# Kernel optimization log

Hardware: AMD Instinct MI355X
Metric: run time of the kernel (lower is better)

Reference implementation:

```python
import jax, jax.numpy as jnp
import numpy as np

# Model constants matching init_kwargs
C1, C2, FS, IMG = 1024, 3, 16, 128
NF = FS * FS                     # n_features = 256 (== pos_out_dim)
L = C1 // NF                     # 4 hypernetwork-generated layers
WD = NF + (L - 1) * NF + L       # weight_dim = 1028
M = NF // 4                      # 64 frequencies per coord dim
SIGMA = 10.0
B = 8


def _coords_pe(b):
    """get_coords([IMG, IMG]) + positional_encoding, flattened to [b, IMG*IMG, NF]."""
    v0, v1 = -0.99999, 1.0
    r = (v1 - v0) / (2 * IMG)
    seq = v0 + r + 2 * r * jnp.arange(IMG, dtype=jnp.float32)
    gy, gx = jnp.meshgrid(seq, seq, indexing='ij')
    coords = jnp.stack([gy, gx], axis=-1)                 # [IMG, IMG, 2]
    j = jnp.arange(M, dtype=jnp.float32)
    coeffs = 2.0 * jnp.pi * (SIGMA ** (j / M))            # [M]
    vp = coeffs * coords[..., None]                       # [IMG, IMG, 2, M]
    pe = jnp.concatenate([jnp.cos(vp), jnp.sin(vp)], -1)  # [IMG, IMG, 2, 2M]
    pe = pe.reshape(IMG, IMG, 4 * M)                      # flatten(-2,-1)
    x2 = pe.reshape(1, IMG * IMG, NF)
    return jnp.broadcast_to(x2, (b, IMG * IMG, NF))


def setup_inputs() -> dict:
    key = jax.random.key(0)
    ks = jax.random.split(key, 5)
    std = 0.001  # matches _initialize_weights
    x = jax.random.normal(ks[0], (B, C1, FS, FS), jnp.float32)
    conv_w = std * jax.random.normal(ks[1], (C1 + L, C1), jnp.float32)  # 1x1 conv kernel
    conv_b = jnp.zeros((C1 + L,), jnp.float32)
    wfine_w = std * jax.random.normal(ks[2], (NF, NF), jnp.float32)
    wfine_b = jnp.zeros((NF,), jnp.float32)
    last1_w = std * jax.random.normal(ks[3], (C2, NF), jnp.float32)
    last1_b = jnp.zeros((C2,), jnp.float32)
    prelu_a = jnp.array(0.25, jnp.float32)  # nn.PReLU default single param
    return {"x": x, "conv_w": conv_w, "conv_b": conv_b,
            "wfine_w": wfine_w, "wfine_b": wfine_b,
            "last1_w": last1_w, "last1_b": last1_b, "prelu_a": prelu_a}


def reference(x, conv_w, conv_b, wfine_w, wfine_b, last1_w, last1_b, prelu_a):
    b = x.shape[0]
    x2 = _coords_pe(b)  # [b, N_px, NF]
    # 1x1 conv == channel matmul
    x1 = jnp.einsum('bchw,oc->bohw', x, conv_w) + conv_b[None, :, None, None]
    W = x1.reshape(b, WD, NF)
    W = jnp.einsum('bik,jk->bij', W, wfine_w) + wfine_b  # W_fine linear
    out = x2
    for j in range(L):
        wj = W[:, NF * j + j: NF * (j + 1) + j, :]           # [b, NF, NF]
        bj = W[:, NF * (j + 1) + j: NF * (j + 1) + j + 1, :]  # [b, 1, NF]
        h = jnp.einsum('bij,bjk->bik', out, wj) + bj
        out = jnp.where(h >= 0, h, prelu_a * h)              # PReLU
    out = jnp.einsum('bik,ck->bic', out, last1_w) + last1_b  # last1
    out = jax.nn.silu(out)                                   # SiLU
    out = out.transpose(0, 2, 1).reshape(b, C2, IMG, IMG)
    return out
```

## Files before the change

kernel.cpp:

```cpp
#include <hip/hip_runtime.h>
#include <hip/hip_fp16.h>
#include <math.h>

typedef _Float16 f16;
typedef _Float16 f16x4 __attribute__((ext_vector_type(4)));
typedef _Float16 f16x8 __attribute__((ext_vector_type(8)));
typedef float f32x4 __attribute__((ext_vector_type(4)));

#define MFMA16(a, b, c) __builtin_amdgcn_mfma_f32_16x16x32_f16((a), (b), (c), 0, 0, 0)

static constexpr float SW_W    = 1024.f;
static constexpr float SA_A    = 64.f;
static constexpr float INV_SW  = 1.f / 1024.f;
static constexpr float INV_SW2 = 1.f / (1024.f * 1024.f);
static constexpr float INV_SASW = 1.f / (64.f * 1024.f);

static constexpr size_t OFF_CY = 0;
static constexpr size_t OFF_CX = OFF_CY + 65536;
static constexpr size_t OFF_LW = OFF_CX + 65536;
static constexpr size_t OFF_S  = OFF_LW + 8192;
static constexpr size_t OFF_CW = OFF_S  + 1024;
static constexpr size_t OFF_M2 = OFF_CW + (size_t)1088 * 1024 * 2;
static constexpr size_t OFF_W  = OFF_M2 + (size_t)8 * 256 * 1024 * 2;
static constexpr size_t OFF_AY = OFF_W  + (size_t)8 * 1028 * 256 * 4;
static constexpr size_t OFF_BX = OFF_AY + (size_t)8 * 128 * 256 * 2;
static constexpr size_t OFF_WT = OFF_BX + (size_t)8 * 128 * 256 * 2;

static __device__ inline f32x4 zero4() { f32x4 v = {0.f, 0.f, 0.f, 0.f}; return v; }

__global__ __launch_bounds__(256, 4) void k_prepA(
    const float* __restrict__ x, const float* __restrict__ wfine,
    f16* __restrict__ M2,
    float* __restrict__ cy, float* __restrict__ cx,
    f16* __restrict__ lwf, const float* __restrict__ lw,
    const float* __restrict__ cw, f16* __restrict__ cw16,
    float* __restrict__ S)
{
    __shared__ __align__(16) f16 Ab[2][64 * 32];
    __shared__ __align__(16) f16 Bb[2][64 * 32];
    const int bid = blockIdx.x;
    const int t = threadIdx.x;
    if (bid < 512) {
        const int lane = t & 63;
        const int wc = t >> 6;
        const int nlo = lane & 15, q4 = lane >> 4;
        const int b = bid >> 6, rem = bid & 63;
        const int jt = rem >> 4, ct = rem & 15;
        const int j0 = jt << 6, c0 = ct << 6;

        auto stageA = [&](int buf, int k0) {
            const float* src = x + (((size_t)((b << 10) + c0 + (t >> 2))) << 8) + k0 + ((t & 3) << 3);
            f16x8 v;
            #pragma unroll
            for (int i = 0; i < 8; i++) v[i] = (f16)src[i];
            *(f16x8*)(&Ab[buf][t << 3]) = v;
        };
        auto stageB = [&](int buf, int k0) {
            const float* src = wfine + (size_t)(j0 + (t >> 2)) * 256 + k0 + ((t & 3) << 3);
            f16x8 v;
            #pragma unroll
            for (int i = 0; i < 8; i++) v[i] = (f16)(src[i] * SW_W);
            *(f16x8*)(&Bb[buf][t << 3]) = v;
        };

        f32x4 acc[4];
        #pragma unroll
        for (int mt = 0; mt < 4; mt++) acc[mt] = zero4();

        stageA(0, 0); stageB(0, 0);
        __syncthreads();
        for (int c = 0; c < 8; c++) {
            const int cb = c & 1;
            if (c + 1 < 8) { stageA(cb ^ 1, (c + 1) << 5); stageB(cb ^ 1, (c + 1) << 5); }
            f16x8 af[4], bf;
            bf = *(const f16x8*)(&Bb[cb][(((wc << 4) + nlo) << 5) + (q4 << 3)]);
            #pragma unroll
            for (int mt = 0; mt < 4; mt++)
                af[mt] = *(const f16x8*)(&Ab[cb][(((mt << 4) + nlo) << 5) + (q4 << 3)]);
            #pragma unroll
            for (int mt = 0; mt < 4; mt++)
                acc[mt] = MFMA16(af[mt], bf, acc[mt]);
            __syncthreads();
        }
        const int j = j0 + (wc << 4) + nlo;
        #pragma unroll
        for (int mt = 0; mt < 4; mt++) {
            const int cc = c0 + (mt << 4) + (q4 << 2);
            f16x4 pk;
            #pragma unroll
            for (int i = 0; i < 4; i++) pk[i] = (f16)acc[mt][i];
            *(f16x4*)(M2 + (((size_t)((b << 8) + j)) << 10) + cc) = pk;
        }
        return;
    }
    if (bid < 642) {
        int id = (bid - 512) * 256 + t;
        const float r = 1.99999f / 256.f;
        if (id < 32768) {
            float* dst = (id < 16384) ? cy : cx;
            int e = id & 16383;
            int row = e >> 7, f = e & 127;
            float s = -0.99999f + r + 2.f * r * (float)row;
            float coef = 6.283185307179586f * powf(10.f, (float)(f & 63) * (1.f / 64.f));
            float arg = coef * s;
            dst[e] = (f < 64) ? cosf(arg) : sinf(arg);
        } else {
            int id2 = id - 32768;
            int c = id2 >> 6, lane = id2 & 63;
            int nlo = lane & 15, q4 = lane >> 4;
            f16x8 v;
            #pragma unroll
            for (int ko = 0; ko < 8; ko++)
                v[ko] = (nlo < 3) ? (f16)(lw[nlo * 256 + (c << 5) + (q4 << 3) + ko] * SW_W) : (f16)0.f;
            *(f16x8*)(lwf + id2 * 8) = v;
        }
        return;
    }
    if (bid < 1186) {
        const int g8 = (bid - 642) * 256 + t;
        const int row = g8 >> 7, col0 = (g8 & 127) << 3;
        f16x8 v;
        if (row < 1028) {
            const float* src = cw + (size_t)row * 1024 + col0;
            #pragma unroll
            for (int i = 0; i < 8; i++) v[i] = (f16)(src[i] * SW_W);
        } else {
            #pragma unroll
            for (int i = 0; i < 8; i++) v[i] = (f16)0.f;
        }
        *(f16x8*)(cw16 + (size_t)g8 * 8) = v;
        return;
    }
    {
        const float* src = wfine + (size_t)t * 256;
        float s = 0.f;
        for (int k = 0; k < 256; k += 4) {
            const f32x4 v = *(const f32x4*)(src + k);
            s += (v[0] + v[1]) + (v[2] + v[3]);
        }
        S[t] = s;
    }
}

__global__ __launch_bounds__(256, 4) void k_gemmB(
    const f16* __restrict__ cw16, const f16* __restrict__ M2,
    const float* __restrict__ conv_b, const float* __restrict__ S,
    const float* __restrict__ wfine_b, float* __restrict__ W)
{
    __shared__ __align__(16) f16 Ab[2][64 * 32];
    __shared__ __align__(16) f16 Bb[2][64 * 32];
    const int t = threadIdx.x;
    const int lane = t & 63;
    const int wc = t >> 6;
    const int nlo = lane & 15, q4 = lane >> 4;
    const int blk = blockIdx.x;
    const int b = blk / 68, rem = blk % 68;
    const int it = rem >> 2, jt = rem & 3;
    const int i0 = it << 6, j0 = jt << 6;

    auto stageA = [&](int buf, int k0) {
        *(f16x8*)(&Ab[buf][t << 3]) =
            *(const f16x8*)(M2 + (((size_t)((b << 8) + j0 + (t >> 2))) << 10) + k0 + ((t & 3) << 3));
    };
    auto stageB = [&](int buf, int k0) {
        *(f16x8*)(&Bb[buf][t << 3]) =
            *(const f16x8*)(cw16 + (((size_t)(i0 + (t >> 2))) << 10) + k0 + ((t & 3) << 3));
    };

    f32x4 acc[4];
    #pragma unroll
    for (int mt = 0; mt < 4; mt++) acc[mt] = zero4();

    stageA(0, 0); stageB(0, 0);
    __syncthreads();
    for (int c = 0; c < 32; c++) {
        const int cb = c & 1;
        if (c + 1 < 32) { stageA(cb ^ 1, (c + 1) << 5); stageB(cb ^ 1, (c + 1) << 5); }
        f16x8 af[4], bf;
        bf = *(const f16x8*)(&Bb[cb][(((wc << 4) + nlo) << 5) + (q4 << 3)]);
        #pragma unroll
        for (int mt = 0; mt < 4; mt++)
            af[mt] = *(const f16x8*)(&Ab[cb][(((mt << 4) + nlo) << 5) + (q4 << 3)]);
        #pragma unroll
        for (int mt = 0; mt < 4; mt++)
            acc[mt] = MFMA16(af[mt], bf, acc[mt]);
        __syncthreads();
    }
    const int i = i0 + (wc << 4) + nlo;
    if (i < 1028) {
        const float cbv = conv_b[i];
        #pragma unroll
        for (int mt = 0; mt < 4; mt++) {
            const int j = j0 + (mt << 4) + (q4 << 2);
            const f32x4 sv = *(const f32x4*)(S + j);
            const f32x4 wb = *(const f32x4*)(wfine_b + j);
            f32x4 o;
            #pragma unroll
            for (int ii = 0; ii < 4; ii++)
                o[ii] = acc[mt][ii] * INV_SW2 + cbv * sv[ii] + wb[ii];
            *(f32x4*)(W + (((size_t)(b * 1028 + i)) << 8) + j) = o;
        }
    }
}

__global__ void k_wprep(const float* __restrict__ cy, const float* __restrict__ cx,
                        const float* __restrict__ W, f16* __restrict__ ayF,
                        f16* __restrict__ bxF, f16* __restrict__ wjT)
{
    __shared__ float tile[64][65];
    const int bid = blockIdx.x;
    const int t = threadIdx.x;
    if (bid < 256) {
        const int b = bid >> 5, which = (bid >> 4) & 1, rtile = bid & 15;
        const int r0 = rtile << 3;
        const float* ctab = which ? cx : cy;
        const float* Wb = W + (size_t)(b * 1028 + (which ? 128 : 0)) * 256;
        float acc[8];
        #pragma unroll
        for (int r = 0; r < 8; r++) acc[r] = 0.f;
        for (int k = 0; k < 128; k++) {
            const float wv = Wb[(k << 8) + t];
            #pragma unroll
            for (int r = 0; r < 8; r++)
                acc[r] = fmaf(ctab[((r0 + r) << 7) + k], wv, acc[r]);
        }
        const float b1v = which ? 0.f : W[(size_t)(b * 1028 + 256) * 256 + t];
        f16* dst = which ? bxF : ayF;
        for (int r = 0; r < 8; r++)
            dst[(size_t)((b << 7) + r0 + r) * 256 + t] = (f16)((acc[r] + b1v) * SA_A);
        return;
    }
    const int id = bid - 256;
    const int b = id / 48;
    const int rr = id % 48;
    const int jj = rr / 16;
    const int tt = rr % 16;
    const int kt = tt >> 2, wt = tt & 3;
    const int k0 = kt << 6, n0 = wt << 6;
    const float* src = W + (size_t)(b * 1028 + 257 * (jj + 1)) * 256;
    for (int i = 0; i < 16; i++) {
        int e = i * 256 + t;
        int kk = e >> 6, nn = e & 63;
        tile[kk][nn] = src[(size_t)(k0 + kk) * 256 + n0 + nn];
    }
    __syncthreads();
    f16* dst = wjT + (size_t)(b * 3 + jj) * 65536;
    #pragma unroll
    for (int i = 0; i < 2; i++) {
        const int g = i * 256 + t;
        const int c_rel = g >> 8, sub = g & 255;
        const int nt = sub >> 6, ln = sub & 63;
        const int nl = ln & 15, q4g = ln >> 4;
        f16x8 v;
        #pragma unroll
        for (int ko = 0; ko < 8; ko++)
            v[ko] = (f16)(tile[(c_rel << 5) + (q4g << 3) + ko][(nt << 4) + nl] * SW_W);
        const int c = (kt << 1) + c_rel;
        *(f16x8*)(dst + (size_t)(((((c << 2) | wt) << 2) | nt) << 9) + (ln << 3)) = v;
    }
}

__global__ __launch_bounds__(256, 3) void k_main(
    const f16* __restrict__ wjT, const float* __restrict__ Wfull,
    const f16* __restrict__ ayF, const f16* __restrict__ bxF,
    const f16* __restrict__ lwf, const float* __restrict__ lb,
    const float* __restrict__ pa_p, float* __restrict__ out)
{
    __shared__ __align__(16) unsigned char actS[32768];
    const int t = threadIdx.x;
    const int lane = t & 63;
    const int wc = t >> 6;
    const int nlo = lane & 15, q4 = lane >> 4;
    const int blk = blockIdx.x;
    const int b = blk & 7, rt = blk >> 3;
    const int p0 = rt << 6;
    const int y = p0 >> 7, x0 = p0 & 127;
    const float pa = pa_p[0];

    const f16* wl0 = wjT + (size_t)(b * 3) * 65536;
    auto loadBg = [&](f16x8* dstv, int g) {
        const f16* p = wl0 + (size_t)(g >> 3) * 65536 + ((size_t)((((g & 7) << 2) | wc)) << 11) + (lane << 3);
        #pragma unroll
        for (int nt = 0; nt < 4; nt++) dstv[nt] = *(const f16x8*)(p + (nt << 9));
    };
    auto lbar = [&]() {
        asm volatile("s_waitcnt lgkmcnt(0)" ::: "memory");
        __builtin_amdgcn_s_barrier();
        __builtin_amdgcn_sched_barrier(0);
    };

    f16x8 bfA[4], bfB[4];
    loadBg(bfA, 0);

    {
        const int r = t & 63, g8 = t >> 6;
        const f16* ayr = ayF + (size_t)((b << 7) + y) * 256;
        const f16* bxr = bxF + (size_t)((b << 7) + x0 + r) * 256;
        const int rx = r & 7;
        #pragma unroll
        for (int mm = 0; mm < 8; mm++) {
            const int slot = (g8 << 3) + mm;
            const int f0 = slot << 3;
            f16x8 av = *(const f16x8*)(ayr + f0);
            f16x8 bv = *(const f16x8*)(bxr + f0);
            f16x8 v;
            #pragma unroll
            for (int i = 0; i < 8; i++) {
                float hv = (float)av[i] + (float)bv[i];
                hv = fmaxf(hv, 0.f) + pa * fminf(hv, 0.f);
                v[i] = (f16)hv;
            }
            *(f16x8*)(actS + (r << 9) + ((slot ^ rx) << 4)) = v;
        }
    }
    lbar();

    for (int jj = 0; jj < 3; jj++) {
        const float* bias = Wfull + (size_t)(b * 1028 + 257 * (jj + 1) + 256) * 256;
        f32x4 bias4[4];
        #pragma unroll
        for (int nt = 0; nt < 4; nt++) {
            bias4[nt] = *(const f32x4*)(bias + (wc << 6) + (nt << 4) + (q4 << 2));
            bias4[nt] *= SA_A;
        }

        f32x4 acc[4][4];
        #pragma unroll
        for (int pt = 0; pt < 4; pt++)
            #pragma unroll
            for (int nt = 0; nt < 4; nt++) acc[pt][nt] = zero4();

        #pragma unroll
        for (int c = 0; c < 8; c++) {
            const int g = jj * 8 + c;
            f16x8* curW = (c & 1) ? bfB : bfA;
            f16x8* nxtW = (c & 1) ? bfA : bfB;
            if (g < 23) loadBg(nxtW, g + 1);
            const int sl = (c << 2) + q4;
            f16x8 af[4];
            #pragma unroll
            for (int pt = 0; pt < 4; pt++) {
                const int rr = (pt << 4) + nlo;
                af[pt] = *(const f16x8*)(actS + (rr << 9) + ((sl ^ (rr & 7)) << 4));
            }
            #pragma unroll
            for (int pt = 0; pt < 4; pt++)
                #pragma unroll
                for (int nt = 0; nt < 4; nt++)
                    acc[pt][nt] = MFMA16(curW[nt], af[pt], acc[pt][nt]);
        }
        lbar();

        #pragma unroll
        for (int nt = 0; nt < 4; nt++) {
            const int nb = (wc << 6) + (nt << 4) + (q4 << 2);
            #pragma unroll
            for (int pt = 0; pt < 4; pt++) {
                const int rr = (pt << 4) + nlo;
                f16x4 pk;
                #pragma unroll
                for (int i = 0; i < 4; i++) {
                    float v = fmaf(acc[pt][nt][i], INV_SW, bias4[nt][i]);
                    v = fmaxf(v, 0.f) + pa * fminf(v, 0.f);
                    pk[i] = (f16)v;
                }
                *(f16x4*)(actS + (rr << 9) + (((nb >> 3) ^ (rr & 7)) << 4) + ((nb & 7) << 1)) = pk;
            }
        }
        lbar();
    }

    {
        f32x4 acc2 = zero4();
        const int rr = (wc << 4) + nlo;
        #pragma unroll
        for (int c = 0; c < 8; c++) {
            const int sl = (c << 2) + q4;
            const f16x8 af = *(const f16x8*)(actS + (rr << 9) + ((sl ^ (rr & 7)) << 4));
            const f16x8 lf = *(const f16x8*)(lwf + (((c << 6) + lane) << 3));
            acc2 = MFMA16(af, lf, acc2);
        }
        if (nlo < 3) {
            const float lbv = lb[nlo];
            float* ob = out + ((size_t)(b * 3 + nlo) << 14) + p0 + (wc << 4) + (q4 << 2);
            #pragma unroll
            for (int i = 0; i < 4; i++) {
                float z = acc2[i] * INV_SASW + lbv;
                ob[i] = z / (1.f + expf(-z));
            }
        }
    }
}

extern "C" void kernel_launch(void* const* d_in, const int* in_sizes, int n_in,
                              void* d_out, int out_size, void* d_ws, size_t ws_size,
                              hipStream_t stream)
{
    (void)in_sizes; (void)n_in; (void)out_size; (void)ws_size;
    const float* x       = (const float*)d_in[0];
    const float* conv_w  = (const float*)d_in[1];
    const float* conv_b  = (const float*)d_in[2];
    const float* wfine_w = (const float*)d_in[3];
    const float* wfine_b = (const float*)d_in[4];
    const float* last1_w = (const float*)d_in[5];
    const float* last1_b = (const float*)d_in[6];
    const float* prelu_a = (const float*)d_in[7];
    char* ws = (char*)d_ws;
    float* Cy  = (float*)(ws + OFF_CY);
    float* Cx  = (float*)(ws + OFF_CX);
    f16*   lwf = (f16*)(ws + OFF_LW);
    float* S   = (float*)(ws + OFF_S);
    f16*   cw16= (f16*)(ws + OFF_CW);
    f16*   M2  = (f16*)(ws + OFF_M2);
    float* W   = (float*)(ws + OFF_W);
    f16*   AyF = (f16*)(ws + OFF_AY);
    f16*   BxF = (f16*)(ws + OFF_BX);
    f16*   wjT = (f16*)(ws + OFF_WT);

    k_prepA<<<1187, 256, 0, stream>>>(x, wfine_w, M2, Cy, Cx, lwf, last1_w, conv_w, cw16, S);
    k_gemmB<<<544, 256, 0, stream>>>(cw16, M2, conv_b, S, wfine_b, W);
    k_wprep<<<640, 256, 0, stream>>>(Cy, Cx, W, AyF, BxF, wjT);
    k_main<<<2048, 256, 0, stream>>>(wjT, W, AyF, BxF, lwf, last1_b, prelu_a, (float*)d_out);
}
```

Baseline: 113.3 us.

## Stage hypernetwork weight tiles through LDS with async global_load_lds triple buffering

Per-wave weight fragments for the generated layers now stream into a three-deep LDS ring via direct global-to-LDS loads, replacing the register double buffer. Waits use vmcnt so up to two tiles stay in flight behind the MFMAs. The change also unrolls the outer layer loop. It adds 48KB of LDS and lowers launch bounds to 2 blocks per CU, trading occupancy for deeper prefetch and less register pressure.

```diff
diff --git a/kernel.cpp b/kernel.cpp
--- a/kernel.cpp
+++ b/kernel.cpp
@@ -260,13 +260,14 @@
     }
 }
 
-__global__ __launch_bounds__(256, 3) void k_main(
+__global__ __launch_bounds__(256, 2) void k_main(
     const f16* __restrict__ wjT, const float* __restrict__ Wfull,
     const f16* __restrict__ ayF, const f16* __restrict__ bxF,
     const f16* __restrict__ lwf, const float* __restrict__ lb,
     const float* __restrict__ pa_p, float* __restrict__ out)
 {
     __shared__ __align__(16) unsigned char actS[32768];
+    __shared__ __align__(16) unsigned char wS[4][3][4096];
     const int t = threadIdx.x;
     const int lane = t & 63;
     const int wc = t >> 6;
@@ -278,10 +279,14 @@
     const float pa = pa_p[0];
 
     const f16* wl0 = wjT + (size_t)(b * 3) * 65536;
-    auto loadBg = [&](f16x8* dstv, int g) {
-        const f16* p = wl0 + (size_t)(g >> 3) * 65536 + ((size_t)((((g & 7) << 2) | wc)) << 11) + (lane << 3);
-        #pragma unroll
-        for (int nt = 0; nt < 4; nt++) dstv[nt] = *(const f16x8*)(p + (nt << 9));
+    auto stage = [&](int g) {
+        const f16* p = wl0 + ((size_t)(g >> 3) << 15) + ((((g & 7) << 2) | wc) << 11) + (lane << 3);
+        const unsigned char* l = wS[wc][g % 3] + (lane << 4);
+        #pragma unroll
+        for (int i = 0; i < 4; i++)
+            __builtin_amdgcn_global_load_lds(
+                (const __attribute__((address_space(1))) void*)(p + (i << 9)),
+                (__attribute__((address_space(3))) void*)(l + (i << 10)), 16, 0, 0);
     };
     auto lbar = [&]() {
         asm volatile("s_waitcnt lgkmcnt(0)" ::: "memory");
@@ -289,8 +294,7 @@
         __builtin_amdgcn_sched_barrier(0);
     };
 
-    f16x8 bfA[4], bfB[4];
-    loadBg(bfA, 0);
+    stage(0); stage(1); stage(2);
 
     {
         const int r = t & 63, g8 = t >> 6;
@@ -315,6 +319,7 @@
     }
     lbar();
 
+    #pragma unroll
     for (int jj = 0; jj < 3; jj++) {
         const float* bias = Wfull + (size_t)(b * 1028 + 257 * (jj + 1) + 256) * 256;
         f32x4 bias4[4];
@@ -333,11 +338,14 @@
         #pragma unroll
         for (int c = 0; c < 8; c++) {
             const int g = jj * 8 + c;
-            f16x8* curW = (c & 1) ? bfB : bfA;
-            f16x8* nxtW = (c & 1) ? bfA : bfB;
-            if (g < 23) loadBg(nxtW, g + 1);
+            asm volatile("s_waitcnt vmcnt(8)" ::: "memory");
+            __builtin_amdgcn_sched_barrier(0);
+            const unsigned char* ws = wS[wc][g % 3];
+            f16x8 bw[4], af[4];
+            #pragma unroll
+            for (int nt = 0; nt < 4; nt++)
+                bw[nt] = *(const f16x8*)(ws + (nt << 10) + (lane << 4));
             const int sl = (c << 2) + q4;
-            f16x8 af[4];
             #pragma unroll
             for (int pt = 0; pt < 4; pt++) {
                 const int rr = (pt << 4) + nlo;
@@ -347,7 +355,9 @@
             for (int pt = 0; pt < 4; pt++)
                 #pragma unroll
                 for (int nt = 0; nt < 4; nt++)
-                    acc[pt][nt] = MFMA16(curW[nt], af[pt], acc[pt][nt]);
+                    acc[pt][nt] = MFMA16(bw[nt], af[pt], acc[pt][nt]);
+            __builtin_amdgcn_sched_barrier(0);
+            if (g + 3 < 24) stage(g + 3);
         }
         lbar();
 
```

Measured after the change: 119.4 us. 5.4% more time.

## Double pixel tile per block to reuse loaded weight fragments across 128 pixels

Applied to the files above, without the earlier changes.

Each block of the main kernel now covers a full 128-pixel image row instead of 64 pixels. Each weight fragment loaded from global memory feeds two accumulator sets, which halves weight traffic per pixel. To fit this, LDS grows to 64KB, the launch bound drops to one block per SM and the grid is halved. The bias loads move after the GEMM loop to save registers. The costs are lower occupancy, higher register pressure and fewer blocks available for load balancing.

```diff
diff --git a/kernel.cpp b/kernel.cpp
--- a/kernel.cpp
+++ b/kernel.cpp
@@ -260,21 +260,21 @@
     }
 }
 
-__global__ __launch_bounds__(256, 3) void k_main(
+__global__ __launch_bounds__(256, 1) void k_main(
     const f16* __restrict__ wjT, const float* __restrict__ Wfull,
     const f16* __restrict__ ayF, const f16* __restrict__ bxF,
     const f16* __restrict__ lwf, const float* __restrict__ lb,
     const float* __restrict__ pa_p, float* __restrict__ out)
 {
-    __shared__ __align__(16) unsigned char actS[32768];
+    __shared__ __align__(16) unsigned char actS[65536];
     const int t = threadIdx.x;
     const int lane = t & 63;
     const int wc = t >> 6;
     const int nlo = lane & 15, q4 = lane >> 4;
     const int blk = blockIdx.x;
     const int b = blk & 7, rt = blk >> 3;
-    const int p0 = rt << 6;
-    const int y = p0 >> 7, x0 = p0 & 127;
+    const int p0 = rt << 7;
+    const int y = rt;
     const float pa = pa_p[0];
 
     const f16* wl0 = wjT + (size_t)(b * 3) * 65536;
@@ -293,13 +293,13 @@
     loadBg(bfA, 0);
 
     {
-        const int r = t & 63, g8 = t >> 6;
+        const int r = t & 127, g8 = t >> 7;
         const f16* ayr = ayF + (size_t)((b << 7) + y) * 256;
-        const f16* bxr = bxF + (size_t)((b << 7) + x0 + r) * 256;
+        const f16* bxr = bxF + (size_t)((b << 7) + r) * 256;
         const int rx = r & 7;
         #pragma unroll
-        for (int mm = 0; mm < 8; mm++) {
-            const int slot = (g8 << 3) + mm;
+        for (int mm = 0; mm < 16; mm++) {
+            const int slot = (g8 << 4) + mm;
             const int f0 = slot << 3;
             f16x8 av = *(const f16x8*)(ayr + f0);
             f16x8 bv = *(const f16x8*)(bxr + f0);
@@ -316,19 +316,11 @@
     lbar();
 
     for (int jj = 0; jj < 3; jj++) {
-        const float* bias = Wfull + (size_t)(b * 1028 + 257 * (jj + 1) + 256) * 256;
-        f32x4 bias4[4];
-        #pragma unroll
-        for (int nt = 0; nt < 4; nt++) {
-            bias4[nt] = *(const f32x4*)(bias + (wc << 6) + (nt << 4) + (q4 << 2));
-            bias4[nt] *= SA_A;
-        }
-
-        f32x4 acc[4][4];
+        f32x4 accA[4][4], accB[4][4];
         #pragma unroll
         for (int pt = 0; pt < 4; pt++)
             #pragma unroll
-            for (int nt = 0; nt < 4; nt++) acc[pt][nt] = zero4();
+            for (int nt = 0; nt < 4; nt++) { accA[pt][nt] = zero4(); accB[pt][nt] = zero4(); }
 
         #pragma unroll
         for (int c = 0; c < 8; c++) {
@@ -337,42 +329,64 @@
             f16x8* nxtW = (c & 1) ? bfA : bfB;
             if (g < 23) loadBg(nxtW, g + 1);
             const int sl = (c << 2) + q4;
-            f16x8 af[4];
+            f16x8 afA[4], afB[4];
             #pragma unroll
             for (int pt = 0; pt < 4; pt++) {
                 const int rr = (pt << 4) + nlo;
-                af[pt] = *(const f16x8*)(actS + (rr << 9) + ((sl ^ (rr & 7)) << 4));
+                afA[pt] = *(const f16x8*)(actS + (rr << 9) + ((sl ^ (rr & 7)) << 4));
             }
             #pragma unroll
             for (int pt = 0; pt < 4; pt++)
                 #pragma unroll
                 for (int nt = 0; nt < 4; nt++)
-                    acc[pt][nt] = MFMA16(curW[nt], af[pt], acc[pt][nt]);
+                    accA[pt][nt] = MFMA16(curW[nt], afA[pt], accA[pt][nt]);
+            #pragma unroll
+            for (int pt = 0; pt < 4; pt++) {
+                const int rr = 64 + (pt << 4) + nlo;
+                afB[pt] = *(const f16x8*)(actS + (rr << 9) + ((sl ^ (rr & 7)) << 4));
+            }
+            #pragma unroll
+            for (int pt = 0; pt < 4; pt++)
+                #pragma unroll
+                for (int nt = 0; nt < 4; nt++)
+                    accB[pt][nt] = MFMA16(curW[nt], afB[pt], accB[pt][nt]);
         }
         lbar();
 
+        const float* bias = Wfull + (size_t)(b * 1028 + 257 * (jj + 1) + 256) * 256;
         #pragma unroll
         for (int nt = 0; nt < 4; nt++) {
             const int nb = (wc << 6) + (nt << 4) + (q4 << 2);
+            const f32x4 b4 = *(const f32x4*)(bias + nb);
             #pragma unroll
             for (int pt = 0; pt < 4; pt++) {
-                const int rr = (pt << 4) + nlo;
-                f16x4 pk;
+                const int rrA = (pt << 4) + nlo;
+                f16x4 pkA;
                 #pragma unroll
                 for (int i = 0; i < 4; i++) {
-                    float v = fmaf(acc[pt][nt][i], INV_SW, bias4[nt][i]);
+                    float v = fmaf(accA[pt][nt][i], INV_SW, b4[i] * SA_A);
                     v = fmaxf(v, 0.f) + pa * fminf(v, 0.f);
-                    pk[i] = (f16)v;
+                    pkA[i] = (f16)v;
                 }
-                *(f16x4*)(actS + (rr << 9) + (((nb >> 3) ^ (rr & 7)) << 4) + ((nb & 7) << 1)) = pk;
+                *(f16x4*)(actS + (rrA << 9) + (((nb >> 3) ^ (rrA & 7)) << 4) + ((nb & 7) << 1)) = pkA;
+                const int rrB = 64 + rrA;
+                f16x4 pkB;
+                #pragma unroll
+                for (int i = 0; i < 4; i++) {
+                    float v = fmaf(accB[pt][nt][i], INV_SW, b4[i] * SA_A);
+                    v = fmaxf(v, 0.f) + pa * fminf(v, 0.f);
+                    pkB[i] = (f16)v;
+                }
+                *(f16x4*)(actS + (rrB << 9) + (((nb >> 3) ^ (rrB & 7)) << 4) + ((nb & 7) << 1)) = pkB;
             }
         }
         lbar();
     }
 
-    {
+    #pragma unroll
+    for (int gi = 0; gi < 2; gi++) {
         f32x4 acc2 = zero4();
-        const int rr = (wc << 4) + nlo;
+        const int rr = (wc << 5) + (gi << 4) + nlo;
         #pragma unroll
         for (int c = 0; c < 8; c++) {
             const int sl = (c << 2) + q4;
@@ -382,7 +396,7 @@
         }
         if (nlo < 3) {
             const float lbv = lb[nlo];
-            float* ob = out + ((size_t)(b * 3 + nlo) << 14) + p0 + (wc << 4) + (q4 << 2);
+            float* ob = out + ((size_t)(b * 3 + nlo) << 14) + p0 + (wc << 5) + (gi << 4) + (q4 << 2);
             #pragma unroll
             for (int i = 0; i < 4; i++) {
                 float z = acc2[i] * INV_SASW + lbv;
@@ -420,5 +434,5 @@
     k_prepA<<<1187, 256, 0, stream>>>(x, wfine_w, M2, Cy, Cx, lwf, last1_w, conv_w, cw16, S);
     k_gemmB<<<544, 256, 0, stream>>>(cw16, M2, conv_b, S, wfine_b, W);
     k_wprep<<<640, 256, 0, stream>>>(Cy, Cx, W, AyF, BxF, wjT);
-    k_main<<<2048, 256, 0, stream>>>(wjT, W, AyF, BxF, lwf, last1_b, prelu_a, (float*)d_out);
+    k_main<<<1024, 256, 0, stream>>>(wjT, W, AyF, BxF, lwf, last1_b, prelu_a, (float*)d_out);
 }
```

New measurement: 131.0 us. 15.7% more time.
